# Performance work log

Hardware: AMD Instinct MI355X
Metric: run time of the kernel (lower is better)

The kernel has to match this reference:

```python
import jax, jax.numpy as jnp
import numpy as np

NUM_CLASSES = 3
EXCEPT_THRESH = 0.05
NMS_THRESH = 0.5
NMS_TOPK = 500
BATCH = 16
ANCHORS_PER_LOC = 3


def _make_scale(key, grid, stride):
    """Build realistic YOLO-style output / anchor / offset / stride tensors for one scale."""
    A = ANCHORS_PER_LOC
    N = grid * grid * A
    out = jax.random.normal(key, (BATCH, N, 5 + NUM_CLASSES), dtype=jnp.float32)
    ys, xs = jnp.meshgrid(jnp.arange(grid, dtype=jnp.float32),
                          jnp.arange(grid, dtype=jnp.float32), indexing='ij')
    off = jnp.stack([xs, ys], axis=-1).reshape(grid * grid, 1, 2)         # (G*G,1,2)
    off = jnp.broadcast_to(off, (grid * grid, A, 2)).reshape(1, N, 2)
    base = jnp.array([[16., 16.], [32., 24.], [24., 48.]], jnp.float32) * (stride / 8.0)
    anc = jnp.broadcast_to(base.reshape(1, 1, A, 2), (1, grid * grid, A, 2)).reshape(1, N, 2)
    st = jnp.full((1, 1, 2), stride, dtype=jnp.float32)
    return out, anc, off, st


def setup_inputs() -> dict:
    key = jax.random.key(0)
    k1, k2, k3 = jax.random.split(key, 3)
    o1, a1, f1, s1 = _make_scale(k1, 96, 8.0)
    o2, a2, f2, s2 = _make_scale(k2, 48, 16.0)
    o3, a3, f3, s3 = _make_scale(k3, 24, 32.0)
    return {
        'output1': o1, 'output2': o2, 'output3': o3,
        'anchor1': a1, 'anchor2': a2, 'anchor3': a3,
        'offset1': f1, 'offset2': f2, 'offset3': f3,
        'stride1': s1, 'stride2': s2, 'stride3': s3,
    }


def _decode(out, anchor, offset, stride):
    """YOLOv3 multiperclass decode -> (B, N*C, 6) rows of [id, score, x1, y1, x2, y2]."""
    xy, wh = out[..., 0:2], out[..., 2:4]
    obj, cls = out[..., 4:5], out[..., 5:]
    # from_sigmoid=False: apply sigmoid to centers / objectness / class logits
    xy = jax.nn.sigmoid(xy)
    obj = jax.nn.sigmoid(obj)
    cls = jax.nn.sigmoid(cls)
    center = (xy + offset) * stride              # (B,N,2)
    half = 0.5 * jnp.exp(wh) * anchor            # (B,N,2)
    bbox = jnp.concatenate([center - half, center + half], axis=-1)  # (B,N,4)
    scores = obj * cls                           # (B,N,C)
    B, N, C = scores.shape
    ids = jnp.broadcast_to(jnp.arange(C, dtype=jnp.float32), (B, N, C))
    mask = scores > EXCEPT_THRESH
    ids = jnp.where(mask, ids, -1.0)
    scr = jnp.where(mask, scores, -1.0)
    bb = jnp.broadcast_to(bbox[:, :, None, :], (B, N, C, 4))
    res = jnp.concatenate([ids[..., None], scr[..., None], bb], axis=-1)
    return res.reshape(B, N * C, 6)


def _iou_matrix(boxes):
    """boxes (K,4) corner format -> (K,K) IoU."""
    x1, y1, x2, y2 = boxes[:, 0], boxes[:, 1], boxes[:, 2], boxes[:, 3]
    area = jnp.maximum(x2 - x1, 0.0) * jnp.maximum(y2 - y1, 0.0)
    iw = jnp.maximum(jnp.minimum(x2[:, None], x2[None]) - jnp.maximum(x1[:, None], x1[None]), 0.0)
    ih = jnp.maximum(jnp.minimum(y2[:, None], y2[None]) - jnp.maximum(y1[:, None], y1[None]), 0.0)
    inter = iw * ih
    return inter / (area[:, None] + area[None] - inter + 1e-12)


def _greedy_keep(iou, valid):
    """Greedy NMS over score-sorted candidates. iou (K,K), valid (K,) -> keep (K,) bool."""
    K = iou.shape[0]
    ar = jnp.arange(K)
    def body(i, keep):
        suppressed = jnp.any(keep & (ar < i) & (iou[i] > NMS_THRESH))
        return keep.at[i].set(valid[i] & ~suppressed)
    return jax.lax.fori_loop(0, K, body, valid)


def _per_class_nms(ids, scores, bboxes):
    """ids/scores (B,M,1), bboxes (B,M,4). Suppressed candidates get id=-1, score=-1.
    uid=-1 (background / below-threshold) entries pass through untouched, matching the
    original which skips NMS for uid<0."""
    B, M = ids.shape[:2]
    idf, scf = ids[..., 0], scores[..., 0]
    scatter = jax.vmap(lambda kf, o, k: kf.at[o].set(k))
    for c in range(NUM_CLASSES):
        cmask = idf == float(c)
        s = jnp.where(cmask, scf, -jnp.inf)
        order = jnp.argsort(-s, axis=1)[:, :NMS_TOPK]            # (B,K)
        sb = jnp.take_along_axis(s, order, axis=1)               # (B,K)
        bb = jnp.take_along_axis(bboxes, order[..., None], axis=1)  # (B,K,4)
        valid = jnp.isfinite(sb)
        iou = jax.vmap(_iou_matrix)(bb)                          # (B,K,K)
        keep = jax.vmap(_greedy_keep)(iou, valid)                # (B,K)
        keep_full = scatter(jnp.zeros((B, M), bool), order, keep)
        sup = cmask & ~keep_full                                 # suppressed or beyond topk
        idf = jnp.where(sup, -1.0, idf)
        scf = jnp.where(sup, -1.0, scf)
    return idf[..., None], scf[..., None], bboxes


def reference(output1, output2, output3, anchor1, anchor2, anchor3,
              offset1, offset2, offset3, stride1, stride2, stride3):
    results = jnp.concatenate([
        _decode(output1, anchor1, offset1, stride1),
        _decode(output2, anchor2, offset2, stride2),
        _decode(output3, anchor3, offset3, stride3),
    ], axis=1)                                   # (B, M, 6)
    ids = results[:, :, 0:1]
    scores = results[:, :, 1:2]
    bboxes = results[:, :, 2:]
    return _per_class_nms(ids, scores, bboxes)
```

## Files before the change

kernel.cpp:

```cpp
#include <hip/hip_runtime.h>

#define N1 27648
#define N2 6912
#define N3 1728
#define NTOT 36288
#define BATCH_ 16
#define C_ 3
#define GRP (BATCH_ * C_)
#define MROWS (NTOT * C_)
#define TOPK 500
#define NBINS 2304
#define CCAP 2048
#define BASEBITS 0x3D400000u
#define TPRE 0.5f
#define LISTCAP 4096
#define CNT_STRIDE 32

#define OFF_LIST   8192ull
#define SZ_LIST    ((size_t)GRP * LISTCAP * 8)
#define OFF_KEYS   (OFF_LIST + SZ_LIST)
#define SZ_KEYS    ((size_t)GRP * 512 * 8)
#define OFF_BOXES  (OFF_KEYS + SZ_KEYS)
#define SZ_BOXES   ((size_t)GRP * 512 * 16)
#define OFF_MASKS  (OFF_BOXES + SZ_BOXES)
#define SZ_MASKS   ((size_t)GRP * 4096 * 8)
#define OFF_KCNT   (OFF_MASKS + SZ_MASKS)
#define SZ_KCNT    4096ull
#define WS_NEED    (OFF_KCNT + SZ_KCNT)

__device__ __forceinline__ float sigm(float x) { return 1.0f / (1.0f + expf(-x)); }

__device__ __forceinline__ float score_of(int b, int n, int c,
    const float* __restrict__ o1, const float* __restrict__ o2, const float* __restrict__ o3)
{
    const float* o; int ln, Ns;
    if (n < N1)           { o = o1; ln = n;             Ns = N1; }
    else if (n < N1 + N2) { o = o2; ln = n - N1;        Ns = N2; }
    else                  { o = o3; ln = n - (N1 + N2); Ns = N3; }
    const float* r = o + ((size_t)b * Ns + ln) * 8;
    return sigm(r[4]) * sigm(r[5 + c]);
}

__device__ __forceinline__ unsigned wave_push(bool pred, unsigned* cntp)
{
    unsigned long long mb = __ballot(pred);
    unsigned pos = 0xFFFFFFFFu;
    if (pred) {
        int lane = threadIdx.x & 63;
        int leader = __ffsll((long long)mb) - 1;
        unsigned total = (unsigned)__popcll(mb);
        unsigned base = 0;
        if (lane == leader) base = atomicAdd(cntp, total);
        base = __shfl(base, leader);
        pos = base + (unsigned)__popcll(mb & ((1ull << lane) - 1ull));
    }
    return pos;
}

#define FILL_N4 (2 * BATCH_ * MROWS / 4)
__global__ __launch_bounds__(256) void fill_kernel(float4* __restrict__ out4,
                                                   unsigned* __restrict__ cnts)
{
    int i = blockIdx.x * 256 + threadIdx.x;
    if (i < FILL_N4) out4[i] = make_float4(-1.0f, -1.0f, -1.0f, -1.0f);
    if (cnts != nullptr && blockIdx.x == 0 && threadIdx.x < GRP)
        cnts[threadIdx.x * CNT_STRIDE] = 0u;
}

__global__ __launch_bounds__(256) void decode_filter_kernel(
    const float* __restrict__ o1, const float* __restrict__ o2, const float* __restrict__ o3,
    const float* __restrict__ a1, const float* __restrict__ a2, const float* __restrict__ a3,
    const float* __restrict__ f1, const float* __restrict__ f2, const float* __restrict__ f3,
    const float* __restrict__ s1, const float* __restrict__ s2, const float* __restrict__ s3,
    float* __restrict__ out,
    unsigned* __restrict__ cnts, unsigned long long* __restrict__ list, int listcap)
{
    __shared__ unsigned lcnt[C_];
    __shared__ unsigned lbase[C_];
    __shared__ unsigned long long stage[C_][256];

    const int tid = threadIdx.x;
    const int n = blockIdx.x * 256 + tid;
    const int b = blockIdx.y;
    const bool active = (n < NTOT);

    if (tid < C_) lcnt[tid] = 0u;
    __syncthreads();

    if (active) {
        const float *o, *anc, *off, *st; int ln, Ns;
        if (n < N1)           { o = o1; anc = a1; off = f1; st = s1; ln = n;             Ns = N1; }
        else if (n < N1 + N2) { o = o2; anc = a2; off = f2; st = s2; ln = n - N1;        Ns = N2; }
        else                  { o = o3; anc = a3; off = f3; st = s3; ln = n - (N1 + N2); Ns = N3; }
        const float* r = o + ((size_t)b * Ns + ln) * 8;
        float4 v0 = *(const float4*)r;
        float4 v1 = *(const float4*)(r + 4);

        float sx = sigm(v0.x);
        float sy = sigm(v0.y);
        float cx = (sx + off[2 * ln + 0]) * st[0];
        float cy = (sy + off[2 * ln + 1]) * st[1];
        float hx = 0.5f * expf(v0.z) * anc[2 * ln + 0];
        float hy = 0.5f * expf(v0.w) * anc[2 * ln + 1];
        float4 bb = make_float4(cx - hx, cy - hy, cx + hx, cy + hy);

        size_t base = (size_t)b * MROWS + (size_t)n * C_;
        float* bbs = out + 2ull * BATCH_ * MROWS;
        float4* bp = (float4*)(bbs + base * 4);
        bp[0] = bb; bp[1] = bb; bp[2] = bb;

        if (listcap > 0) {
            float sobj = sigm(v1.x);
            float s[3] = { sobj * sigm(v1.y), sobj * sigm(v1.z), sobj * sigm(v1.w) };
            #pragma unroll
            for (int c = 0; c < C_; ++c) {
                if (s[c] > TPRE) {
                    unsigned p = atomicAdd(&lcnt[c], 1u);
                    stage[c][p] =
                        ((unsigned long long)__float_as_uint(s[c]) << 32) | (unsigned)(~n);
                }
            }
        }
    }

    if (listcap > 0) {
        __syncthreads();
        if (tid < C_)
            lbase[tid] = atomicAdd(&cnts[(b * C_ + tid) * CNT_STRIDE], lcnt[tid]);
        __syncthreads();
        #pragma unroll
        for (int c = 0; c < C_; ++c) {
            unsigned m = lcnt[c];
            if ((unsigned)tid < m) {
                unsigned pos = lbase[c] + (unsigned)tid;
                if (pos < (unsigned)listcap)
                    list[(size_t)(b * C_ + c) * listcap + pos] = stage[c][tid];
            }
        }
    }
}

__global__ __launch_bounds__(512) void topk_kernel(
    const float* __restrict__ o1, const float* __restrict__ o2, const float* __restrict__ o3,
    const float* __restrict__ out,
    const unsigned* __restrict__ cnts, const unsigned long long* __restrict__ list,
    unsigned long long* __restrict__ gkeys, float4* __restrict__ gboxes,
    unsigned* __restrict__ kcnt)
{
    const int g = blockIdx.x;
    const int b = g / C_;
    const int c = g - b * C_;
    const int tid = threadIdx.x;

    __shared__ unsigned long long keys[CCAP];
    __shared__ unsigned int hist[NBINS];
    __shared__ unsigned int sh_tb, sh_cnt;

    unsigned cnt_g = cnts[g * CNT_STRIDE];
    const bool pathL = (cnt_g >= TOPK && cnt_g <= (unsigned)LISTCAP);
    const unsigned long long* L = list + (size_t)g * LISTCAP;

    for (int i = tid; i < NBINS; i += 512) hist[i] = 0u;
    if (tid == 0) sh_cnt = 0u;
    __syncthreads();

    if (pathL) {
        for (unsigned i = tid; i < cnt_g; i += 512) {
            unsigned bin = ((unsigned)(L[i] >> 32) - BASEBITS) >> 14;
            if (bin > NBINS - 1u) bin = NBINS - 1u;
            atomicAdd(&hist[bin], 1u);
        }
    } else {
        for (int n = tid; n < NTOT; n += 512) {
            float s = score_of(b, n, c, o1, o2, o3);
            if (s > 0.05f) {
                unsigned bin = (__float_as_uint(s) - BASEBITS) >> 14;
                if (bin > NBINS - 1u) bin = NBINS - 1u;
                atomicAdd(&hist[bin], 1u);
            }
        }
    }
    __syncthreads();

    if (tid < 64) {
        const int CHUNK = NBINS / 64;
        int base_i = tid * CHUNK;
        unsigned own = 0;
        #pragma unroll
        for (int k = 0; k < CHUNK; ++k) own += hist[base_i + k];
        unsigned sfx = own;
        #pragma unroll
        for (int off = 1; off < 64; off <<= 1) {
            unsigned v = __shfl_down(sfx, off, 64);
            sfx += (tid + off < 64) ? v : 0u;
        }
        unsigned sfxn = sfx - own;
        if (tid == 0 && sfx < TOPK) sh_tb = 0u;
        if (sfx >= TOPK && sfxn < TOPK) {
            unsigned cum = sfxn, tb = (unsigned)base_i;
            for (int k = CHUNK - 1; k >= 0; --k) {
                cum += hist[base_i + k];
                if (cum >= TOPK) { tb = (unsigned)(base_i + k); break; }
            }
            sh_tb = tb;
        }
    }
    __syncthreads();

    const unsigned tb = sh_tb;
    if (pathL) {
        unsigned nIter = (cnt_g + 511u) & ~511u;
        for (unsigned i = tid; i < nIter; i += 512) {
            bool pred = false; unsigned long long key = 0ull;
            if (i < cnt_g) {
                key = L[i];
                unsigned bin = ((unsigned)(key >> 32) - BASEBITS) >> 14;
                if (bin > NBINS - 1u) bin = NBINS - 1u;
                pred = (bin >= tb);
            }
            unsigned p = wave_push(pred, &sh_cnt);
            if (pred && p < CCAP) keys[p] = key;
        }
    } else {
        const int nIter = (NTOT + 511) & ~511;
        for (int n = tid; n < nIter; n += 512) {
            bool pred = false; unsigned long long key = 0ull;
            if (n < NTOT) {
                float s = score_of(b, n, c, o1, o2, o3);
                if (s > 0.05f) {
                    unsigned bits = __float_as_uint(s);
                    unsigned bin = (bits - BASEBITS) >> 14;
                    if (bin > NBINS - 1u) bin = NBINS - 1u;
                    if (bin >= tb) {
                        pred = true;
                        key = ((unsigned long long)bits << 32) | (unsigned)(~n);
                    }
                }
            }
            unsigned p = wave_push(pred, &sh_cnt);
            if (pred && p < CCAP) keys[p] = key;
        }
    }
    __syncthreads();

    const unsigned cnt2 = min(sh_cnt, (unsigned)CCAP);
    unsigned S2 = 2;
    while (S2 < cnt2) S2 <<= 1;
    for (unsigned i = tid; i < S2; i += 512)
        if (i >= cnt2) keys[i] = 0ull;
    __syncthreads();

    for (unsigned k = 2; k <= S2; k <<= 1) {
        for (unsigned j = k >> 1; j > 0; j >>= 1) {
            for (unsigned i = tid; i < S2; i += 512) {
                unsigned ixj = i ^ j;
                if (ixj > i) {
                    unsigned long long x = keys[i], y = keys[ixj];
                    bool desc = ((i & k) == 0);
                    if (desc ? (x < y) : (x > y)) { keys[i] = y; keys[ixj] = x; }
                }
            }
            __syncthreads();
        }
    }

    const int K = (int)min(cnt2, (unsigned)TOPK);

    if (tid == 0) kcnt[g] = (unsigned)K;
    if (tid < K) {
        unsigned long long key = keys[tid];
        gkeys[(size_t)g * 512 + tid] = key;
        unsigned idx = ~(unsigned)(key & 0xFFFFFFFFull);
        const float* bbs = out + 2ull * BATCH_ * MROWS;
        gboxes[(size_t)g * 512 + tid] =
            *(const float4*)(bbs + ((size_t)b * MROWS + (size_t)idx * C_) * 4);
    }
}

__global__ __launch_bounds__(256) void masks_kernel(
    const float4* __restrict__ gboxes, const unsigned* __restrict__ kcnt,
    unsigned long long* __restrict__ gmasks)
{
    const int g = blockIdx.x;
    const int w = blockIdx.y;
    const int K = (int)kcnt[g];

    __shared__ float bx[TOPK * 4];
    __shared__ float ar[TOPK];

    const float4* B = gboxes + (size_t)g * 512;
    for (int j = threadIdx.x; j < K; j += 256) {
        float4 v = B[j];
        bx[j*4+0] = v.x; bx[j*4+1] = v.y; bx[j*4+2] = v.z; bx[j*4+3] = v.w;
        ar[j] = fmaxf(v.z - v.x, 0.0f) * fmaxf(v.w - v.y, 0.0f);
    }
    __syncthreads();

    unsigned long long* M = gmasks + (size_t)g * 4096 + (size_t)w * 512;
    const int j0 = w * 64;
    const int jhi = (K < j0 + 64) ? K : j0 + 64;

    for (int i = threadIdx.x; i < K; i += 256) {
        unsigned long long word = 0ull;
        if (i + 1 < jhi) {
            float xi1 = bx[i*4+0], yi1 = bx[i*4+1], xi2 = bx[i*4+2], yi2 = bx[i*4+3];
            float ai = ar[i];
            for (int j = j0; j < jhi; ++j) {
                float xj1 = bx[j*4+0], yj1 = bx[j*4+1], xj2 = bx[j*4+2], yj2 = bx[j*4+3];
                float aj = ar[j];
                float iw = fmaxf(fminf(xi2, xj2) - fmaxf(xi1, xj1), 0.0f);
                float ih = fmaxf(fminf(yi2, yj2) - fmaxf(yi1, yj1), 0.0f);
                float inter = iw * ih;
                float iou = inter / (ai + aj - inter + 1e-12f);
                if (iou > 0.5f && j > i) word |= 1ull << (j - j0);
            }
        }
        M[i] = word;
    }
}

__global__ __launch_bounds__(512) void greedy_kernel(
    const unsigned long long* __restrict__ gmasks,
    const unsigned long long* __restrict__ gkeys,
    const unsigned* __restrict__ kcnt, float* __restrict__ out)
{
    const int g = blockIdx.x;
    const int b = g / C_;
    const int c = g - b * C_;
    const int tid = threadIdx.x;
    const int K = (int)kcnt[g];

    __shared__ unsigned long long mlds[512 * 9];
    __shared__ unsigned long long keep_s[8];

    const unsigned long long* GM = gmasks + (size_t)g * 4096;
    for (int t = tid; t < 8 * 512; t += 512) {
        int w = t >> 9, i = t & 511;
        mlds[i * 9 + w] = (i < K) ? GM[w * 512 + i] : 0ull;
    }
    __syncthreads();

    if (tid < 64) {
        const int lane8 = tid & 7;
        unsigned long long removed = 0ull, keep = 0ull;
        const int Kpad = (K + 7) & ~7;

        unsigned long long m0 = mlds[0*9+lane8], m1 = mlds[1*9+lane8],
                           m2 = mlds[2*9+lane8], m3 = mlds[3*9+lane8],
                           m4 = mlds[4*9+lane8], m5 = mlds[5*9+lane8],
                           m6 = mlds[6*9+lane8], m7 = mlds[7*9+lane8];

        for (int i0 = 0; i0 < Kpad; i0 += 8) {
            int nb = (i0 + 8 < 512) ? (i0 + 8) : 0;
            unsigned long long n0 = mlds[(nb+0)*9+lane8], n1 = mlds[(nb+1)*9+lane8],
                               n2 = mlds[(nb+2)*9+lane8], n3 = mlds[(nb+3)*9+lane8],
                               n4 = mlds[(nb+4)*9+lane8], n5 = mlds[(nb+5)*9+lane8],
                               n6 = mlds[(nb+6)*9+lane8], n7 = mlds[(nb+7)*9+lane8];

            #define GSTEP(t, mt) { \
                int i = i0 + t; \
                int w = i >> 6, bp = i & 63; \
                bool mine = (tid == w) && ((removed >> bp) & 1ull); \
                unsigned long long alive = __any(mine) ? 0ull : ~0ull; \
                keep |= ((tid == w) ? (1ull << bp) : 0ull) & alive; \
                removed |= mt & alive; \
            }
            GSTEP(0, m0) GSTEP(1, m1) GSTEP(2, m2) GSTEP(3, m3)
            GSTEP(4, m4) GSTEP(5, m5) GSTEP(6, m6) GSTEP(7, m7)
            #undef GSTEP

            m0=n0; m1=n1; m2=n2; m3=n3; m4=n4; m5=n5; m6=n6; m7=n7;
        }
        if (tid < 8) keep_s[tid] = keep;
    }
    __syncthreads();

    const unsigned long long* GK = gkeys + (size_t)g * 512;
    for (int i = tid; i < K; i += 512) {
        if ((keep_s[i >> 6] >> (i & 63)) & 1ull) {
            unsigned long long key = GK[i];
            unsigned idx = ~(unsigned)(key & 0xFFFFFFFFull);
            float sc = __uint_as_float((unsigned)(key >> 32));
            size_t row = (size_t)b * MROWS + (size_t)idx * C_ + c;
            out[row] = (float)c;
            out[(size_t)BATCH_ * MROWS + row] = sc;
        }
    }
}

__global__ __launch_bounds__(512) void select_nms_mono(
    const float* __restrict__ o1, const float* __restrict__ o2, const float* __restrict__ o3,
    float* __restrict__ out,
    const unsigned* __restrict__ cnts, const unsigned long long* __restrict__ list, int listcap)
{
    const int g = blockIdx.x;
    const int b = g / C_;
    const int c = g - b * C_;
    const int tid = threadIdx.x;

    __shared__ unsigned long long smem[7048];
    __shared__ unsigned int sh_tb, sh_cnt;
    __shared__ unsigned long long keepw[8];

    unsigned long long* keys = smem;
    unsigned int* hist = (unsigned int*)(smem + CCAP);
    float* boxes = (float*)(smem + CCAP);
    unsigned long long* masks = smem + 3048;

    unsigned cnt_g = 0;
    bool pathL = false;
    if (listcap >= TOPK) {
        cnt_g = cnts[g * CNT_STRIDE];
        pathL = (cnt_g >= TOPK && cnt_g <= (unsigned)listcap);
    }
    const unsigned long long* L = list + (size_t)g * (size_t)(listcap > 0 ? listcap : 1);

    for (int i = tid; i < NBINS; i += 512) hist[i] = 0u;
    if (tid == 0) sh_cnt = 0u;
    __syncthreads();

    if (pathL) {
        for (unsigned i = tid; i < cnt_g; i += 512) {
            unsigned bin = ((unsigned)(L[i] >> 32) - BASEBITS) >> 14;
            if (bin > NBINS - 1u) bin = NBINS - 1u;
            atomicAdd(&hist[bin], 1u);
        }
    } else {
        for (int n = tid; n < NTOT; n += 512) {
            float s = score_of(b, n, c, o1, o2, o3);
            if (s > 0.05f) {
                unsigned bin = (__float_as_uint(s) - BASEBITS) >> 14;
                if (bin > NBINS - 1u) bin = NBINS - 1u;
                atomicAdd(&hist[bin], 1u);
            }
        }
    }
    __syncthreads();

    if (tid < 64) {
        const int CHUNK = NBINS / 64;
        int base_i = tid * CHUNK;
        unsigned own = 0;
        #pragma unroll
        for (int k = 0; k < CHUNK; ++k) own += hist[base_i + k];
        unsigned sfx = own;
        #pragma unroll
        for (int off = 1; off < 64; off <<= 1) {
            unsigned v = __shfl_down(sfx, off, 64);
            sfx += (tid + off < 64) ? v : 0u;
        }
        unsigned sfxn = sfx - own;
        if (tid == 0 && sfx < TOPK) sh_tb = 0u;
        if (sfx >= TOPK && sfxn < TOPK) {
            unsigned cum = sfxn, tb = (unsigned)base_i;
            for (int k = CHUNK - 1; k >= 0; --k) {
                cum += hist[base_i + k];
                if (cum >= TOPK) { tb = (unsigned)(base_i + k); break; }
            }
            sh_tb = tb;
        }
    }
    __syncthreads();

    const unsigned tb = sh_tb;
    if (pathL) {
        for (unsigned i = tid; i < cnt_g; i += 512) {
            unsigned long long key = L[i];
            unsigned bin = ((unsigned)(key >> 32) - BASEBITS) >> 14;
            if (bin > NBINS - 1u) bin = NBINS - 1u;
            if (bin >= tb) {
                unsigned p = atomicAdd(&sh_cnt, 1u);
                if (p < CCAP) keys[p] = key;
            }
        }
    } else {
        for (int n = tid; n < NTOT; n += 512) {
            float s = score_of(b, n, c, o1, o2, o3);
            if (s > 0.05f) {
                unsigned bits = __float_as_uint(s);
                unsigned bin = (bits - BASEBITS) >> 14;
                if (bin > NBINS - 1u) bin = NBINS - 1u;
                if (bin >= tb) {
                    unsigned p = atomicAdd(&sh_cnt, 1u);
                    if (p < CCAP)
                        keys[p] = ((unsigned long long)bits << 32) | (unsigned)(~n);
                }
            }
        }
    }
    __syncthreads();

    const unsigned cnt2 = min(sh_cnt, (unsigned)CCAP);
    unsigned S2 = 2;
    while (S2 < cnt2) S2 <<= 1;
    for (unsigned i = tid; i < S2; i += 512)
        if (i >= cnt2) keys[i] = 0ull;
    __syncthreads();

    for (unsigned k = 2; k <= S2; k <<= 1) {
        for (unsigned j = k >> 1; j > 0; j >>= 1) {
            for (unsigned i = tid; i < S2; i += 512) {
                unsigned ixj = i ^ j;
                if (ixj > i) {
                    unsigned long long x = keys[i], y = keys[ixj];
                    bool desc = ((i & k) == 0);
                    if (desc ? (x < y) : (x > y)) { keys[i] = y; keys[ixj] = x; }
                }
            }
            __syncthreads();
        }
    }

    const int K = (int)min(cnt2, (unsigned)TOPK);

    {
        const float* bbs = out + 2ull * BATCH_ * MROWS;
        if (tid < K) {
            unsigned idx = ~(unsigned)(keys[tid] & 0xFFFFFFFFull);
            float4 bb = *(const float4*)(bbs + ((size_t)b * MROWS + (size_t)idx * C_) * 4);
            ((float4*)boxes)[tid] = bb;
        }
    }
    __syncthreads();

    {
        const int nw = (K + 63) >> 6;
        for (int t = tid; t < K * nw; t += 512) {
            int w = t / K;
            int i = t - w * K;
            float xi1 = boxes[i*4+0], yi1 = boxes[i*4+1], xi2 = boxes[i*4+2], yi2 = boxes[i*4+3];
            float ai = fmaxf(xi2 - xi1, 0.0f) * fmaxf(yi2 - yi1, 0.0f);
            unsigned long long word = 0ull;
            int jlo = (i + 1 > w * 64) ? i + 1 : w * 64;
            int jhi = (K < (w + 1) * 64) ? K : (w + 1) * 64;
            for (int j = jlo; j < jhi; ++j) {
                float xj1 = boxes[j*4+0], yj1 = boxes[j*4+1], xj2 = boxes[j*4+2], yj2 = boxes[j*4+3];
                float aj = fmaxf(xj2 - xj1, 0.0f) * fmaxf(yj2 - yj1, 0.0f);
                float iw = fmaxf(fminf(xi2, xj2) - fmaxf(xi1, xj1), 0.0f);
                float ih = fmaxf(fminf(yi2, yj2) - fmaxf(yi1, yj1), 0.0f);
                float inter = iw * ih;
                float iou = inter / (ai + aj - inter + 1e-12f);
                if (iou > 0.5f) word |= 1ull << (j & 63);
            }
            masks[i * 8 + w] = word;
        }
    }
    __syncthreads();

    if (tid < 64) {
        unsigned long long removed = 0ull, keep = 0ull;
        for (int i = 0; i < K; ++i) {
            unsigned long long mw = (tid < 8) ? masks[i * 8 + tid] : 0ull;
            int w = i >> 6, bp = i & 63;
            bool mine = (tid == w) && ((removed >> bp) & 1ull);
            if (!__any(mine)) {
                if (tid == w) keep |= 1ull << bp;
                removed |= mw;
            }
        }
        if (tid < 8) keepw[tid] = keep;
    }
    __syncthreads();

    if (tid < K && ((keepw[tid >> 6] >> (tid & 63)) & 1ull)) {
        unsigned long long key = keys[tid];
        unsigned idx = ~(unsigned)(key & 0xFFFFFFFFull);
        float sc = __uint_as_float((unsigned)(key >> 32));
        size_t row = (size_t)b * MROWS + (size_t)idx * C_ + c;
        out[row] = (float)c;
        out[(size_t)BATCH_ * MROWS + row] = sc;
    }
}

extern "C" void kernel_launch(void* const* d_in, const int* in_sizes, int n_in,
                              void* d_out, int out_size, void* d_ws, size_t ws_size,
                              hipStream_t stream)
{
    const float* o1 = (const float*)d_in[0];
    const float* o2 = (const float*)d_in[1];
    const float* o3 = (const float*)d_in[2];
    const float* a1 = (const float*)d_in[3];
    const float* a2 = (const float*)d_in[4];
    const float* a3 = (const float*)d_in[5];
    const float* f1 = (const float*)d_in[6];
    const float* f2 = (const float*)d_in[7];
    const float* f3 = (const float*)d_in[8];
    const float* s1 = (const float*)d_in[9];
    const float* s2 = (const float*)d_in[10];
    const float* s3 = (const float*)d_in[11];
    float* out = (float*)d_out;

    unsigned* cnts = (unsigned*)d_ws;
    const bool haveCnts = (ws_size >= (size_t)GRP * CNT_STRIDE * 4);

    fill_kernel<<<dim3((FILL_N4 + 255) / 256), dim3(256), 0, stream>>>(
        (float4*)out, haveCnts ? cnts : nullptr);

    if (ws_size >= WS_NEED) {
        unsigned long long* list   = (unsigned long long*)((char*)d_ws + OFF_LIST);
        unsigned long long* gkeys  = (unsigned long long*)((char*)d_ws + OFF_KEYS);
        float4*             gboxes = (float4*)((char*)d_ws + OFF_BOXES);
        unsigned long long* gmasks = (unsigned long long*)((char*)d_ws + OFF_MASKS);
        unsigned*           kcnt   = (unsigned*)((char*)d_ws + OFF_KCNT);

        decode_filter_kernel<<<dim3((NTOT + 255) / 256, BATCH_), dim3(256), 0, stream>>>(
            o1, o2, o3, a1, a2, a3, f1, f2, f3, s1, s2, s3, out, cnts, list, LISTCAP);
        topk_kernel<<<dim3(GRP), dim3(512), 0, stream>>>(
            o1, o2, o3, out, cnts, list, gkeys, gboxes, kcnt);
        masks_kernel<<<dim3(GRP, 8), dim3(256), 0, stream>>>(gboxes, kcnt, gmasks);
        greedy_kernel<<<dim3(GRP), dim3(512), 0, stream>>>(gmasks, gkeys, kcnt, out);
    } else {
        unsigned long long* list = (unsigned long long*)((char*)d_ws + OFF_LIST);
        int listcap = 0;
        if (haveCnts && ws_size >= OFF_LIST + (size_t)GRP * TOPK * 8) {
            size_t cap = (ws_size - OFF_LIST) / (8ull * GRP);
            listcap = (int)(cap > LISTCAP ? LISTCAP : cap);
        }
        decode_filter_kernel<<<dim3((NTOT + 255) / 256, BATCH_), dim3(256), 0, stream>>>(
            o1, o2, o3, a1, a2, a3, f1, f2, f3, s1, s2, s3, out, cnts, list, listcap);
        select_nms_mono<<<dim3(GRP), dim3(512), 0, stream>>>(
            o1, o2, o3, out, cnts, list, listcap);
    }
}
```

Measured before the change: 95.95 us.

## Fuse output fill into decode kernel with nontemporal stores

Removes the separate fill kernel that wrote -1 over the whole ids/scores/bboxes output. The decode kernel now writes the -1 ids and scores for each row itself, alongside the box rows, using nontemporal stores. A tiny kernel now only zeroes the counters. The change also adds unroll pragmas to the list-scan loops in topk. Correctness now relies on the decode kernel covering every row, and on later kernels writing kept rows after decode finishes.

```diff
diff --git a/kernel.cpp b/kernel.cpp
--- a/kernel.cpp
+++ b/kernel.cpp
@@ -28,6 +28,8 @@
 #define SZ_KCNT    4096ull
 #define WS_NEED    (OFF_KCNT + SZ_KCNT)
 
+typedef float f4_t __attribute__((ext_vector_type(4)));
+
 __device__ __forceinline__ float sigm(float x) { return 1.0f / (1.0f + expf(-x)); }
 
 __device__ __forceinline__ float score_of(int b, int n, int c,
@@ -57,14 +59,9 @@
     return pos;
 }
 
-#define FILL_N4 (2 * BATCH_ * MROWS / 4)
-__global__ __launch_bounds__(256) void fill_kernel(float4* __restrict__ out4,
-                                                   unsigned* __restrict__ cnts)
-{
-    int i = blockIdx.x * 256 + threadIdx.x;
-    if (i < FILL_N4) out4[i] = make_float4(-1.0f, -1.0f, -1.0f, -1.0f);
-    if (cnts != nullptr && blockIdx.x == 0 && threadIdx.x < GRP)
-        cnts[threadIdx.x * CNT_STRIDE] = 0u;
+__global__ __launch_bounds__(64) void zerocnt_kernel(unsigned* __restrict__ cnts)
+{
+    if (threadIdx.x < GRP) cnts[threadIdx.x * CNT_STRIDE] = 0u;
 }
 
 __global__ __launch_bounds__(256) void decode_filter_kernel(
@@ -102,12 +99,24 @@
         float cy = (sy + off[2 * ln + 1]) * st[1];
         float hx = 0.5f * expf(v0.z) * anc[2 * ln + 0];
         float hy = 0.5f * expf(v0.w) * anc[2 * ln + 1];
-        float4 bb = make_float4(cx - hx, cy - hy, cx + hx, cy + hy);
+        f4_t bb = { cx - hx, cy - hy, cx + hx, cy + hy };
 
         size_t base = (size_t)b * MROWS + (size_t)n * C_;
+        float* ids = out;
+        float* scs = out + (size_t)BATCH_ * MROWS;
         float* bbs = out + 2ull * BATCH_ * MROWS;
-        float4* bp = (float4*)(bbs + base * 4);
-        bp[0] = bb; bp[1] = bb; bp[2] = bb;
+
+        __builtin_nontemporal_store(-1.0f, &ids[base + 0]);
+        __builtin_nontemporal_store(-1.0f, &ids[base + 1]);
+        __builtin_nontemporal_store(-1.0f, &ids[base + 2]);
+        __builtin_nontemporal_store(-1.0f, &scs[base + 0]);
+        __builtin_nontemporal_store(-1.0f, &scs[base + 1]);
+        __builtin_nontemporal_store(-1.0f, &scs[base + 2]);
+
+        f4_t* bp = (f4_t*)(bbs + base * 4);
+        __builtin_nontemporal_store(bb, bp + 0);
+        __builtin_nontemporal_store(bb, bp + 1);
+        __builtin_nontemporal_store(bb, bp + 2);
 
         if (listcap > 0) {
             float sobj = sigm(v1.x);
@@ -165,6 +174,7 @@
     __syncthreads();
 
     if (pathL) {
+        #pragma unroll 4
         for (unsigned i = tid; i < cnt_g; i += 512) {
             unsigned bin = ((unsigned)(L[i] >> 32) - BASEBITS) >> 14;
             if (bin > NBINS - 1u) bin = NBINS - 1u;
@@ -210,6 +220,7 @@
     const unsigned tb = sh_tb;
     if (pathL) {
         unsigned nIter = (cnt_g + 511u) & ~511u;
+        #pragma unroll 4
         for (unsigned i = tid; i < nIter; i += 512) {
             bool pred = false; unsigned long long key = 0ull;
             if (i < cnt_g) {
@@ -593,8 +604,8 @@
     unsigned* cnts = (unsigned*)d_ws;
     const bool haveCnts = (ws_size >= (size_t)GRP * CNT_STRIDE * 4);
 
-    fill_kernel<<<dim3((FILL_N4 + 255) / 256), dim3(256), 0, stream>>>(
-        (float4*)out, haveCnts ? cnts : nullptr);
+    if (haveCnts)
+        zerocnt_kernel<<<dim3(1), dim3(64), 0, stream>>>(cnts);
 
     if (ws_size >= WS_NEED) {
         unsigned long long* list   = (unsigned long long*)((char*)d_ws + OFF_LIST);
```

Measured after the change: 100.3 us. +4.5%, slower.
